# Optimization experiments

Measured on AMD Instinct MI355X. Metric: run time of the kernel, lower is better.

The kernel has to match this reference:

```python
import jax, jax.numpy as jnp
import numpy as np

D_MODEL = 1024
HEADS = 16
D_K = D_MODEL // HEADS
D_FF = 4096
B, S = 2, 2048
EPS = 1e-5


def setup_inputs() -> dict:
    key = jax.random.key(0)
    ks = jax.random.split(key, 16)
    sc_att = 1.0 / np.sqrt(D_MODEL)
    sc_ff1 = 1.0 / np.sqrt(D_MODEL)
    sc_ff2 = 1.0 / np.sqrt(D_FF)
    return {
        "input": jax.random.normal(ks[0], (B, S, D_MODEL), jnp.float32),
        "mask": jnp.ones((B, 1, 1, S), jnp.int32),
        # stacked per-head projections: [H, D_MODEL, D_K]
        "Wq": jax.random.normal(ks[1], (HEADS, D_MODEL, D_K), jnp.float32) * sc_att,
        "bq": jax.random.normal(ks[2], (HEADS, D_K), jnp.float32) * 0.01,
        "Wk": jax.random.normal(ks[3], (HEADS, D_MODEL, D_K), jnp.float32) * sc_att,
        "bk": jax.random.normal(ks[4], (HEADS, D_K), jnp.float32) * 0.01,
        "Wv": jax.random.normal(ks[5], (HEADS, D_MODEL, D_K), jnp.float32) * sc_att,
        "bv": jax.random.normal(ks[6], (HEADS, D_K), jnp.float32) * 0.01,
        "Wo": jax.random.normal(ks[7], (D_MODEL, D_MODEL), jnp.float32) * sc_att,
        "bo": jax.random.normal(ks[8], (D_MODEL,), jnp.float32) * 0.01,
        "ln1_g": jnp.ones((D_MODEL,), jnp.float32),
        "ln1_b": jnp.zeros((D_MODEL,), jnp.float32),
        "ln2_g": jnp.ones((D_MODEL,), jnp.float32),
        "ln2_b": jnp.zeros((D_MODEL,), jnp.float32),
        "W1": jax.random.normal(ks[9], (D_MODEL, D_FF), jnp.float32) * sc_ff1,
        "b1": jax.random.normal(ks[10], (D_FF,), jnp.float32) * 0.01,
        "W2": jax.random.normal(ks[11], (D_FF, D_MODEL), jnp.float32) * sc_ff2,
        "b2": jax.random.normal(ks[12], (D_MODEL,), jnp.float32) * 0.01,
    }


def _layernorm(x, g, b):
    mu = jnp.mean(x, axis=-1, keepdims=True)
    var = jnp.mean(jnp.square(x - mu), axis=-1, keepdims=True)
    return (x - mu) * jax.lax.rsqrt(var + EPS) * g + b


def reference(input, mask, Wq, bq, Wk, bk, Wv, bv, Wo, bo,
              ln1_g, ln1_b, ln2_g, ln2_b, W1, b1, W2, b2):
    x = input
    # per-head projections, stacked: [B,H,S,D_K]
    q = jnp.einsum('bsd,hdk->bhsk', x, Wq) + bq[None, :, None, :]
    k = jnp.einsum('bsd,hdk->bhsk', x, Wk) + bk[None, :, None, :]
    v = jnp.einsum('bsd,hdk->bhsk', x, Wv) + bv[None, :, None, :]
    scores = jnp.einsum('bhqk,bhsk->bhqs', q, k) / np.sqrt(D_K)  # [B,H,S,S]
    scores = jnp.where(mask == 0, jnp.float32(-1e9), scores)
    attn = jax.nn.softmax(scores, axis=-1)
    ctx = jnp.einsum('bhqs,bhsk->bhqk', attn, v)  # [B,H,S,D_K]
    # concat heads along feature dim (head h occupies slice h*D_K:(h+1)*D_K)
    ctx = jnp.transpose(ctx, (0, 2, 1, 3)).reshape(B, S, D_MODEL)
    att_out = ctx @ Wo + bo
    h = _layernorm(x + att_out, ln1_g, ln1_b)
    ff = jax.nn.relu(h @ W1 + b1) @ W2 + b2
    return _layernorm(h + ff, ln2_g, ln2_b)
```

## Files before the change

kernel.cpp:

```cpp
#include <hip/hip_runtime.h>
#include <cstdint>
#include <cstddef>

typedef unsigned short u16;
typedef unsigned int   u32;
typedef unsigned short u16x4 __attribute__((ext_vector_type(4)));
typedef unsigned short u16x8 __attribute__((ext_vector_type(8)));
typedef unsigned int   u32x2 __attribute__((ext_vector_type(2)));
typedef __bf16 bf16x8 __attribute__((ext_vector_type(8)));
typedef float f32x4 __attribute__((ext_vector_type(4)));

#define MFMA16(a, b, c) __builtin_amdgcn_mfma_f32_16x16x32_bf16((a), (b), (c), 0, 0, 0)

__device__ __forceinline__ float bf2f(u16 h) {
  union { unsigned u; float f; } v; v.u = ((unsigned)h) << 16; return v.f;
}
__device__ __forceinline__ u16 f2bf(float f) {
  union { float f; unsigned u; } v; v.f = f;
  unsigned r = v.u + 0x7fffu + ((v.u >> 16) & 1u);
  return (u16)(r >> 16);
}
__device__ __forceinline__ void gll16(const u16* g, u16* l) {
  __builtin_amdgcn_global_load_lds(
      (const __attribute__((address_space(1))) void*)g,
      (__attribute__((address_space(3))) void*)l, 16, 0, 0);
}
__device__ __forceinline__ float fast_exp2(float x) {
#if __has_builtin(__builtin_amdgcn_exp2f)
  return __builtin_amdgcn_exp2f(x);
#else
  return exp2f(x);
#endif
}

__global__ __launch_bounds__(256) void prep_all(
    const float* __restrict__ bq, const float* __restrict__ bk,
    const float* __restrict__ bv, const int* __restrict__ mask,
    float* __restrict__ biasq, float* __restrict__ madd2,
    const float* __restrict__ x, u16* __restrict__ xb,
    const float* __restrict__ Wq, const float* __restrict__ Wk,
    const float* __restrict__ Wv, u16* __restrict__ Wqkv_t,
    const float* __restrict__ Wo, const float* __restrict__ W1,
    const float* __restrict__ W2, u16* __restrict__ Wo_t,
    u16* __restrict__ W1_t, u16* __restrict__ W2_t) {
  __shared__ u16 tile[32][33];
  const int id = blockIdx.x;
  const int tid = threadIdx.x;

  if (id < 28) {
    int i = id * 256 + tid;
    if (i < 3072) {
      biasq[i] = (i < 1024) ? bq[i] * 0.18033688f
                            : (i < 2048 ? bk[i - 1024] : bv[i - 2048]);
    } else if (i < 7168) {
      int j = i - 3072;
      madd2[j] = mask[j] ? -23.083120f : -1.442695e9f;
    }
    return;
  }
  if (id < 4124) {
    int i = ((id - 28) * 256 + tid) * 4;
    const float4 v = *(const float4*)&x[i];
    u16x4 o;
    o[0] = f2bf(v.x); o[1] = f2bf(v.y); o[2] = f2bf(v.z); o[3] = f2bf(v.w);
    *(u16x4*)&xb[i] = o;
    return;
  }
  if (id < 7196) {
    int t = id - 4124;
    const int bx = t & 1, by = (t >> 1) & 31, z = t >> 6;
    const int which = z >> 4, h = z & 15;
    const float* in = (which == 0 ? Wq : (which == 1 ? Wk : Wv)) + (size_t)h * 1024 * 64;
    u16* out = Wqkv_t + ((size_t)which * 1024 + h * 64) * 1024;
    const float sc = (which == 0) ? 0.18033688f : 1.0f;
    const int tx = tid & 31, ty = tid >> 5;
    const int r0 = by * 32, c0 = bx * 32;
    #pragma unroll
    for (int i = 0; i < 32; i += 8)
      tile[ty + i][tx] = f2bf(in[(size_t)(r0 + ty + i) * 64 + c0 + tx] * sc);
    __syncthreads();
    #pragma unroll
    for (int i = 0; i < 32; i += 8)
      out[(size_t)(c0 + ty + i) * 1024 + r0 + tx] = tile[tx][ty + i];
    return;
  }
  {
    int t0 = id - 7196;
    const float* in; u16* outp; int R, C, cx, ry;
    if (t0 < 1024)      { in = Wo; outp = Wo_t; R = 1024; C = 1024; cx = t0 & 31;  ry = t0 >> 5; }
    else if (t0 < 5120) { int t = t0 - 1024; in = W1; outp = W1_t; R = 1024; C = 4096; cx = t & 127; ry = t >> 7; }
    else                { int t = t0 - 5120; in = W2; outp = W2_t; R = 4096; C = 1024; cx = t & 31;  ry = t >> 5; }
    const int tx = tid & 31, ty = tid >> 5;
    const int r0 = ry * 32, c0 = cx * 32;
    #pragma unroll
    for (int i = 0; i < 32; i += 8)
      tile[ty + i][tx] = f2bf(in[(size_t)(r0 + ty + i) * C + c0 + tx]);
    __syncthreads();
    #pragma unroll
    for (int i = 0; i < 32; i += 8)
      outp[(size_t)(c0 + ty + i) * R + r0 + tx] = tile[tx][ty + i];
  }
}

__device__ __forceinline__ void xcd_tiles(int& m0, int& n0) {
  const int gX = gridDim.x, gY = gridDim.y;
  int n = blockIdx.y * gX + blockIdx.x;
  int cpx = (gX * gY) >> 3;
  int t = (n & 7) * cpx + (n >> 3);
  n0 = (t / gY) * 128;
  m0 = (t % gY) * 128;
}

template <int MODE>
__global__ __launch_bounds__(256) void gemm_bt(
    const u16* __restrict__ A, const u16* __restrict__ Bt,
    const float* __restrict__ bias, u16* __restrict__ C,
    int M, int N, int K) {
  __shared__ __align__(16) u16 As[2][128 * 32];
  __shared__ __align__(16) u16 Bs[2][128 * 32];
  const int tid = threadIdx.x;
  const int lane = tid & 63;
  const int wave = tid >> 6;
  int m0, n0;
  xcd_tiles(m0, n0);
  const int wr = (wave >> 1) * 64;
  const int wc = (wave & 1) * 64;
  const int lrow = lane & 15;
  const int quad = lane >> 4;

  const int srow = lane >> 2;
  const int scol = (lane & 3) * 8;
  const u16* gA1 = &A[(size_t)(m0 + wave * 16 + srow) * K + scol];
  const u16* gA2 = &A[(size_t)(m0 + 64 + wave * 16 + srow) * K + scol];
  const u16* gB1 = &Bt[(size_t)(n0 + wave * 16 + srow) * K + scol];
  const u16* gB2 = &Bt[(size_t)(n0 + 64 + wave * 16 + srow) * K + scol];
  const int so1 = (wave * 16) * 32;
  const int so2 = (wave * 16 + 64) * 32;

  f32x4 acc[4][4];
  #pragma unroll
  for (int i = 0; i < 4; ++i)
    #pragma unroll
    for (int j = 0; j < 4; ++j)
      acc[i][j] = (f32x4){0.f, 0.f, 0.f, 0.f};

  for (int k0 = 0; k0 < K; k0 += 64) {
    gll16(gA1 + k0, &As[0][so1]);
    gll16(gA2 + k0, &As[0][so2]);
    gll16(gB1 + k0, &Bs[0][so1]);
    gll16(gB2 + k0, &Bs[0][so2]);
    gll16(gA1 + k0 + 32, &As[1][so1]);
    gll16(gA2 + k0 + 32, &As[1][so2]);
    gll16(gB1 + k0 + 32, &Bs[1][so1]);
    gll16(gB2 + k0 + 32, &Bs[1][so2]);
    __syncthreads();
    #pragma unroll
    for (int kb = 0; kb < 2; ++kb) {
      bf16x8 af[4], bfr[4];
      #pragma unroll
      for (int i = 0; i < 4; ++i) {
        af[i]  = *(const bf16x8*)&As[kb][(wr + i * 16 + lrow) * 32 + quad * 8];
        bfr[i] = *(const bf16x8*)&Bs[kb][(wc + i * 16 + lrow) * 32 + quad * 8];
      }
      #pragma unroll
      for (int fr = 0; fr < 4; ++fr)
        #pragma unroll
        for (int fc = 0; fc < 4; ++fc)
          acc[fr][fc] = MFMA16(af[fr], bfr[fc], acc[fr][fc]);
    }
    __syncthreads();
  }

  #pragma unroll
  for (int fr = 0; fr < 4; ++fr) {
    int rowb = m0 + wr + fr * 16 + quad * 4;
    #pragma unroll
    for (int fc = 0; fc < 4; ++fc) {
      int col = n0 + wc + fc * 16 + lrow;
      float bv = bias[col];
      #pragma unroll
      for (int r = 0; r < 4; ++r) {
        float v = acc[fr][fc][r] + bv;
        if (MODE == 1) v = fmaxf(v, 0.f);
        C[(size_t)(rowb + r) * N + col] = f2bf(v);
      }
    }
  }
}

__global__ __launch_bounds__(256) void gemm_splitk(
    const u16* __restrict__ A, const u16* __restrict__ Bt,
    u16* __restrict__ Cp, int M, int N, int K) {
  __shared__ __align__(16) u16 As[2][128 * 32];
  __shared__ __align__(16) u16 Bs[2][128 * 32];
  const int tid = threadIdx.x;
  const int lane = tid & 63;
  const int wave = tid >> 6;
  int m0, n0;
  xcd_tiles(m0, n0);
  const int kz = blockIdx.z;
  const int Kh = K >> 1;
  const int kbase = kz * Kh;
  const int wr = (wave >> 1) * 64;
  const int wc = (wave & 1) * 64;
  const int lrow = lane & 15;
  const int quad = lane >> 4;

  const int srow = lane >> 2;
  const int scol = (lane & 3) * 8;
  const u16* gA1 = &A[(size_t)(m0 + wave * 16 + srow) * K + kbase + scol];
  const u16* gA2 = &A[(size_t)(m0 + 64 + wave * 16 + srow) * K + kbase + scol];
  const u16* gB1 = &Bt[(size_t)(n0 + wave * 16 + srow) * K + kbase + scol];
  const u16* gB2 = &Bt[(size_t)(n0 + 64 + wave * 16 + srow) * K + kbase + scol];
  const int so1 = (wave * 16) * 32;
  const int so2 = (wave * 16 + 64) * 32;
  u16* C = Cp + (size_t)kz * M * N;

  f32x4 acc[4][4];
  #pragma unroll
  for (int i = 0; i < 4; ++i)
    #pragma unroll
    for (int j = 0; j < 4; ++j)
      acc[i][j] = (f32x4){0.f, 0.f, 0.f, 0.f};

  for (int k0 = 0; k0 < Kh; k0 += 64) {
    gll16(gA1 + k0, &As[0][so1]);
    gll16(gA2 + k0, &As[0][so2]);
    gll16(gB1 + k0, &Bs[0][so1]);
    gll16(gB2 + k0, &Bs[0][so2]);
    gll16(gA1 + k0 + 32, &As[1][so1]);
    gll16(gA2 + k0 + 32, &As[1][so2]);
    gll16(gB1 + k0 + 32, &Bs[1][so1]);
    gll16(gB2 + k0 + 32, &Bs[1][so2]);
    __syncthreads();
    #pragma unroll
    for (int kb = 0; kb < 2; ++kb) {
      bf16x8 af[4], bfr[4];
      #pragma unroll
      for (int i = 0; i < 4; ++i) {
        af[i]  = *(const bf16x8*)&As[kb][(wr + i * 16 + lrow) * 32 + quad * 8];
        bfr[i] = *(const bf16x8*)&Bs[kb][(wc + i * 16 + lrow) * 32 + quad * 8];
      }
      #pragma unroll
      for (int fr = 0; fr < 4; ++fr)
        #pragma unroll
        for (int fc = 0; fc < 4; ++fc)
          acc[fr][fc] = MFMA16(af[fr], bfr[fc], acc[fr][fc]);
    }
    __syncthreads();
  }

  #pragma unroll
  for (int fr = 0; fr < 4; ++fr) {
    int rowb = m0 + wr + fr * 16 + quad * 4;
    #pragma unroll
    for (int fc = 0; fc < 4; ++fc) {
      int col = n0 + wc + fc * 16 + lrow;
      #pragma unroll
      for (int r = 0; r < 4; ++r)
        C[(size_t)(rowb + r) * N + col] = f2bf(acc[fr][fc][r]);
    }
  }
}

__global__ __launch_bounds__(256) void attn_kernel(
    const u16* __restrict__ xqkv, const float* __restrict__ madd2,
    u16* __restrict__ ctx) {
  __shared__ __align__(16) u16 Ks[128][72];
  __shared__ __align__(16) u16 Vt[64][136];
  __shared__ __align__(16) u16 Ps[4][2][16][72];
  const int tid = threadIdx.x;
  const int lane = tid & 63;
  const int wave = tid >> 6;
  const int lrow = lane & 15;
  const int quad = lane >> 4;
  const int b = blockIdx.z, h = blockIdx.y;
  const int qb = blockIdx.x * 128 + wave * 16;
  const u16* Qp = xqkv + (size_t)b * 2048 * 3072 + h * 64;
  const u16* Kp = Qp + 1024;
  const u16* Vp = Qp + 2048;

  bf16x8 qa[2][2];
  #pragma unroll
  for (int t = 0; t < 2; ++t) {
    qa[t][0] = *(const bf16x8*)&Qp[(size_t)(qb + t * 64 + lrow) * 3072 + quad * 8];
    qa[t][1] = *(const bf16x8*)&Qp[(size_t)(qb + t * 64 + lrow) * 3072 + 32 + quad * 8];
  }

  f32x4 o[2][4];
  #pragma unroll
  for (int t = 0; t < 2; ++t)
    #pragma unroll
    for (int i = 0; i < 4; ++i) o[t][i] = (f32x4){0.f, 0.f, 0.f, 0.f};
  float rsum[2] = {0.f, 0.f};

  const int ks_row = tid >> 3, ks_col = (tid & 7) * 8;
  const int v_dg = tid >> 4;
  const int v_kp = tid & 15;
  const float* maddb = madd2 + b * 2048;

  u16x8 kreg[4];
  u16x4 va[4], vb[4];
  #pragma unroll
  for (int sh = 0; sh < 4; ++sh) {
    kreg[sh] = *(const u16x8*)&Kp[(size_t)(sh * 32 + ks_row) * 3072 + ks_col];
    va[sh] = *(const u16x4*)&Vp[(size_t)(sh * 32 + 2 * v_kp) * 3072 + v_dg * 4];
    vb[sh] = *(const u16x4*)&Vp[(size_t)(sh * 32 + 2 * v_kp + 1) * 3072 + v_dg * 4];
  }

  for (int s0 = 0; s0 < 2048; s0 += 128) {
    __syncthreads();
    #pragma unroll
    for (int sh = 0; sh < 4; ++sh) {
      *(u16x8*)&Ks[sh * 32 + ks_row][ks_col] = kreg[sh];
      #pragma unroll
      for (int j = 0; j < 4; ++j) {
        u32 pk = ((u32)vb[sh][j] << 16) | (u32)va[sh][j];
        *(u32*)&Vt[v_dg * 4 + j][sh * 32 + 2 * v_kp] = pk;
      }
    }
    __syncthreads();
    if (s0 + 128 < 2048) {
      #pragma unroll
      for (int sh = 0; sh < 4; ++sh) {
        int sb = s0 + 128 + sh * 32;
        kreg[sh] = *(const u16x8*)&Kp[(size_t)(sb + ks_row) * 3072 + ks_col];
        va[sh] = *(const u16x4*)&Vp[(size_t)(sb + 2 * v_kp) * 3072 + v_dg * 4];
        vb[sh] = *(const u16x4*)&Vp[(size_t)(sb + 2 * v_kp + 1) * 3072 + v_dg * 4];
      }
    }

    #pragma unroll
    for (int h2 = 0; h2 < 2; ++h2) {
      bf16x8 kf[4][2], vf[4][2];
      #pragma unroll
      for (int kb = 0; kb < 4; ++kb) {
        kf[kb][0] = *(const bf16x8*)&Ks[h2 * 64 + kb * 16 + lrow][quad * 8];
        kf[kb][1] = *(const bf16x8*)&Ks[h2 * 64 + kb * 16 + lrow][32 + quad * 8];
      }
      #pragma unroll
      for (int nb = 0; nb < 4; ++nb) {
        vf[nb][0] = *(const bf16x8*)&Vt[nb * 16 + lrow][(h2 * 2 + 0) * 32 + quad * 8];
        vf[nb][1] = *(const bf16x8*)&Vt[nb * 16 + lrow][(h2 * 2 + 1) * 32 + quad * 8];
      }

      #pragma unroll
      for (int t = 0; t < 2; ++t) {
        #pragma unroll
        for (int kb = 0; kb < 4; ++kb) {
          f32x4 z = (f32x4){0.f, 0.f, 0.f, 0.f};
          z = MFMA16(kf[kb][0], qa[t][0], z);
          z = MFMA16(kf[kb][1], qa[t][1], z);
          f32x4 m4 = *(const f32x4*)&maddb[s0 + h2 * 64 + kb * 16 + quad * 4];
          u32 pb[4];
          #pragma unroll
          for (int r = 0; r < 4; ++r) {
            float p = fast_exp2(z[r] + m4[r]);
            rsum[t] += p;
            union { float f; u32 u; } cv; cv.f = p;
            pb[r] = cv.u + 0x8000u;
          }
          u32x2 w2;
          w2[0] = __builtin_amdgcn_perm(pb[1], pb[0], 0x07060302);
          w2[1] = __builtin_amdgcn_perm(pb[3], pb[2], 0x07060302);
          *(u32x2*)&Ps[wave][t][lrow][kb * 16 + quad * 4] = w2;
        }
        #pragma unroll
        for (int kh = 0; kh < 2; ++kh) {
          bf16x8 pa = *(const bf16x8*)&Ps[wave][t][lrow][kh * 32 + quad * 8];
          #pragma unroll
          for (int nb = 0; nb < 4; ++nb)
            o[t][nb] = MFMA16(pa, vf[nb][kh], o[t][nb]);
        }
      }
    }
  }

  #pragma unroll
  for (int t = 0; t < 2; ++t) {
    float rs = rsum[t];
    rs += __shfl_xor(rs, 16, 64);
    rs += __shfl_xor(rs, 32, 64);
    float inv = 1.f / fmaxf(rs, 1e-30f);
    #pragma unroll
    for (int r = 0; r < 4; ++r) {
      float invq = __shfl(inv, quad * 4 + r, 64);
      int q = qb + t * 64 + quad * 4 + r;
      #pragma unroll
      for (int nb = 0; nb < 4; ++nb) {
        float v = o[t][nb][r] * invq;
        ctx[((size_t)b * 2048 + q) * 1024 + h * 64 + nb * 16 + lrow] = f2bf(v);
      }
    }
  }
}

template <int IN_BF, int OUT_BF>
__global__ __launch_bounds__(256) void add_ln2p(
    const void* __restrict__ xa_, const u16* __restrict__ p0,
    const u16* __restrict__ p1, const float* __restrict__ cb,
    const float* __restrict__ g, const float* __restrict__ bb,
    void* __restrict__ outp_) {
  __shared__ float red[8];
  const int tid = threadIdx.x;
  const size_t base = (size_t)blockIdx.x * 1024;
  const float* xf = (const float*)xa_;
  const u16*   xb = (const u16*)xa_;
  float v[4];
  float s = 0.f;
  #pragma unroll
  for (int i = 0; i < 4; ++i) {
    int c = i * 256 + tid;
    float xv = IN_BF ? bf2f(xb[base + c]) : xf[base + c];
    v[i] = xv + bf2f(p0[base + c]) + bf2f(p1[base + c]) + cb[c];
    s += v[i];
  }
  #pragma unroll
  for (int off = 32; off > 0; off >>= 1) s += __shfl_down(s, off, 64);
  if ((tid & 63) == 0) red[tid >> 6] = s;
  __syncthreads();
  float mean = (red[0] + red[1] + red[2] + red[3]) * (1.f / 1024.f);
  float s2 = 0.f;
  #pragma unroll
  for (int i = 0; i < 4; ++i) { float d = v[i] - mean; s2 += d * d; }
  #pragma unroll
  for (int off = 32; off > 0; off >>= 1) s2 += __shfl_down(s2, off, 64);
  if ((tid & 63) == 0) red[4 + (tid >> 6)] = s2;
  __syncthreads();
  float var = (red[4] + red[5] + red[6] + red[7]) * (1.f / 1024.f);
  float rstd = rsqrtf(var + 1e-5f);
  #pragma unroll
  for (int i = 0; i < 4; ++i) {
    int c = i * 256 + tid;
    float r = (v[i] - mean) * rstd * g[c] + bb[c];
    if (OUT_BF) ((u16*)outp_)[base + c] = f2bf(r);
    else        ((float*)outp_)[base + c] = r;
  }
}

extern "C" void kernel_launch(void* const* d_in, const int* in_sizes, int n_in,
                              void* d_out, int out_size, void* d_ws, size_t ws_size,
                              hipStream_t stream) {
  (void)in_sizes; (void)n_in; (void)out_size; (void)ws_size;
  const float* x    = (const float*)d_in[0];
  const int*   mask = (const int*)d_in[1];
  const float* Wq   = (const float*)d_in[2];
  const float* bq   = (const float*)d_in[3];
  const float* Wk   = (const float*)d_in[4];
  const float* bk   = (const float*)d_in[5];
  const float* Wv   = (const float*)d_in[6];
  const float* bv   = (const float*)d_in[7];
  const float* Wo   = (const float*)d_in[8];
  const float* bo   = (const float*)d_in[9];
  const float* ln1g = (const float*)d_in[10];
  const float* ln1b = (const float*)d_in[11];
  const float* ln2g = (const float*)d_in[12];
  const float* ln2b = (const float*)d_in[13];
  const float* W1   = (const float*)d_in[14];
  const float* b1   = (const float*)d_in[15];
  const float* W2   = (const float*)d_in[16];
  const float* b2   = (const float*)d_in[17];
  float* out = (float*)d_out;

  char* ws = (char*)d_ws;
  u16*   Wqkv_t = (u16*)(ws + 0);
  u16*   fp     = (u16*)(ws + 0);
  u16*   Wo_t   = (u16*)(ws + 6291456);
  u16*   W1_t   = (u16*)(ws + 8388608);
  u16*   W2_t   = (u16*)(ws + 16777216);
  u16*   xqkv   = (u16*)(ws + 25165824);
  u16*   wp     = (u16*)(ws + 25165824);
  u16*   xb     = (u16*)(ws + 50331648);
  u16*   ctx    = (u16*)(ws + 50331648);
  u16*   ff1    = (u16*)(ws + 25165824);
  u16*   hbuf   = (u16*)(ws + 67108864);
  float* biasq  = (float*)(ws + 75497472);
  float* madd2  = (float*)(ws + 75509760);

  prep_all<<<16412, 256, 0, stream>>>(bq, bk, bv, mask, biasq, madd2,
                                      x, xb, Wq, Wk, Wv, Wqkv_t,
                                      Wo, W1, W2, Wo_t, W1_t, W2_t);

  gemm_bt<0><<<dim3(24, 32), 256, 0, stream>>>(xb, Wqkv_t, biasq, xqkv,
                                               4096, 3072, 1024);
  attn_kernel<<<dim3(16, 16, 2), 256, 0, stream>>>(xqkv, madd2, ctx);
  gemm_splitk<<<dim3(8, 32, 2), 256, 0, stream>>>(ctx, Wo_t, wp, 4096, 1024, 1024);
  add_ln2p<0, 1><<<4096, 256, 0, stream>>>(x, wp, wp + 4194304, bo,
                                           ln1g, ln1b, hbuf);
  gemm_bt<1><<<dim3(32, 32), 256, 0, stream>>>(hbuf, W1_t, b1, ff1,
                                               4096, 4096, 1024);
  gemm_splitk<<<dim3(8, 32, 2), 256, 0, stream>>>(ff1, W2_t, fp, 4096, 1024, 4096);
  add_ln2p<1, 0><<<4096, 256, 0, stream>>>(hbuf, fp, fp + 4194304, b2,
                                           ln2g, ln2b, out);
}
```

Measured before the change: 411.2 us.

## Use 256x256 double-buffered GEMM tiles and shrink attention KV tile to 64

Replaces the 128x128 GEMM used for the QKV and FF1 projections with a 512-thread 256x256-tile kernel. It uses 128KB of dynamic LDS double-buffering, interleaves next-tile global-to-LDS loads with MFMA work under barriers, and uses fewer blocks. Separately, the attention kernel now streams K/V in 64-row chunks instead of 128, cutting LDS and register footprint at the cost of more synchronizations per pass. The large tiles raise data reuse but give fewer workgroups: 192 blocks for QKV, 256 for FF1, on a chip with 256 CUs. The 128KB of LDS per block may also limit occupancy.

Result: faster. 366.4 us (-10.9%).

```diff
diff --git a/kernel.cpp b/kernel.cpp
--- a/kernel.cpp
+++ b/kernel.cpp
@@ -110,69 +110,97 @@
   n0 = (t / gY) * 128;
   m0 = (t % gY) * 128;
 }
+__device__ __forceinline__ void xcd_tiles256(int& m0, int& n0) {
+  const int gX = gridDim.x, gY = gridDim.y;
+  int n = blockIdx.y * gX + blockIdx.x;
+  int cpx = (gX * gY) >> 3;
+  int t = (n & 7) * cpx + (n >> 3);
+  n0 = (t / gY) * 256;
+  m0 = (t % gY) * 256;
+}
 
 template <int MODE>
-__global__ __launch_bounds__(256) void gemm_bt(
+__global__ __launch_bounds__(512, 2) void gemm256(
     const u16* __restrict__ A, const u16* __restrict__ Bt,
     const float* __restrict__ bias, u16* __restrict__ C,
     int M, int N, int K) {
-  __shared__ __align__(16) u16 As[2][128 * 32];
-  __shared__ __align__(16) u16 Bs[2][128 * 32];
+  extern __shared__ __align__(16) u16 lds[];
+  u16* As = lds;
+  u16* Bs = lds + 2 * 256 * 64;
   const int tid = threadIdx.x;
-  const int lane = tid & 63;
-  const int wave = tid >> 6;
+  const int lane = tid & 63, wave = tid >> 6;
   int m0, n0;
-  xcd_tiles(m0, n0);
-  const int wr = (wave >> 1) * 64;
-  const int wc = (wave & 1) * 64;
-  const int lrow = lane & 15;
-  const int quad = lane >> 4;
-
-  const int srow = lane >> 2;
-  const int scol = (lane & 3) * 8;
-  const u16* gA1 = &A[(size_t)(m0 + wave * 16 + srow) * K + scol];
-  const u16* gA2 = &A[(size_t)(m0 + 64 + wave * 16 + srow) * K + scol];
-  const u16* gB1 = &Bt[(size_t)(n0 + wave * 16 + srow) * K + scol];
-  const u16* gB2 = &Bt[(size_t)(n0 + 64 + wave * 16 + srow) * K + scol];
-  const int so1 = (wave * 16) * 32;
-  const int so2 = (wave * 16 + 64) * 32;
-
-  f32x4 acc[4][4];
-  #pragma unroll
-  for (int i = 0; i < 4; ++i)
+  xcd_tiles256(m0, n0);
+  const int wr = (wave >> 2) * 128;
+  const int wc = (wave & 3) * 64;
+  const int lrow = lane & 15, quad = lane >> 4;
+
+  const int g_r = wave * 8 + (lane >> 3);
+  const int g_c = (lane & 7) * 8;
+  const u16* gA = A + (size_t)(m0 + g_r) * K + g_c;
+  const u16* gB = Bt + (size_t)(n0 + g_r) * K + g_c;
+  const int wbase = wave * 512;
+
+  f32x4 acc[8][4];
+  #pragma unroll
+  for (int i = 0; i < 8; ++i)
     #pragma unroll
     for (int j = 0; j < 4; ++j)
       acc[i][j] = (f32x4){0.f, 0.f, 0.f, 0.f};
 
-  for (int k0 = 0; k0 < K; k0 += 64) {
-    gll16(gA1 + k0, &As[0][so1]);
-    gll16(gA2 + k0, &As[0][so2]);
-    gll16(gB1 + k0, &Bs[0][so1]);
-    gll16(gB2 + k0, &Bs[0][so2]);
-    gll16(gA1 + k0 + 32, &As[1][so1]);
-    gll16(gA2 + k0 + 32, &As[1][so2]);
-    gll16(gB1 + k0 + 32, &Bs[1][so1]);
-    gll16(gB2 + k0 + 32, &Bs[1][so2]);
-    __syncthreads();
-    #pragma unroll
-    for (int kb = 0; kb < 2; ++kb) {
-      bf16x8 af[4], bfr[4];
-      #pragma unroll
-      for (int i = 0; i < 4; ++i) {
-        af[i]  = *(const bf16x8*)&As[kb][(wr + i * 16 + lrow) * 32 + quad * 8];
-        bfr[i] = *(const bf16x8*)&Bs[kb][(wc + i * 16 + lrow) * 32 + quad * 8];
-      }
-      #pragma unroll
-      for (int fr = 0; fr < 4; ++fr)
+  const int NT = K >> 6;
+
+  #pragma unroll
+  for (int h = 0; h < 2; ++h) {
+    gll16(gA + (size_t)(h * 128) * K,      As + h * 8192 + wbase);
+    gll16(gA + (size_t)(h * 128 + 64) * K, As + h * 8192 + 4096 + wbase);
+    gll16(gB + (size_t)(h * 128) * K,      Bs + h * 8192 + wbase);
+    gll16(gB + (size_t)(h * 128 + 64) * K, Bs + h * 8192 + 4096 + wbase);
+  }
+  __syncthreads();
+
+  for (int t = 0; t < NT; ++t) {
+    const int p = t & 1;
+    const u16* Ab = As + p * 16384;
+    const u16* Bb = Bs + p * 16384;
+    bf16x8 bfr[4][2];
+    #pragma unroll
+    for (int q = 0; q < 4; ++q) {
+      if (q == 0) {
         #pragma unroll
         for (int fc = 0; fc < 4; ++fc)
-          acc[fr][fc] = MFMA16(af[fr], bfr[fc], acc[fr][fc]);
-    }
-    __syncthreads();
-  }
-
-  #pragma unroll
-  for (int fr = 0; fr < 4; ++fr) {
+          #pragma unroll
+          for (int kh = 0; kh < 2; ++kh)
+            bfr[fc][kh] = *(const bf16x8*)&Bb[(wc + fc * 16 + lrow) * 64 + kh * 32 + quad * 8];
+      }
+      bf16x8 af2[2][2];
+      #pragma unroll
+      for (int j = 0; j < 2; ++j)
+        #pragma unroll
+        for (int kh = 0; kh < 2; ++kh)
+          af2[j][kh] = *(const bf16x8*)&Ab[(wr + (q * 2 + j) * 16 + lrow) * 64 + kh * 32 + quad * 8];
+      if (t + 1 < NT) {
+        const int kc = (t + 1) * 64;
+        u16* dst = ((q < 2) ? As : Bs) + (p ^ 1) * 16384 + (q & 1) * 8192 + wbase;
+        const u16* src = ((q < 2) ? gA : gB) + (size_t)((q & 1) * 128) * K + kc;
+        gll16(src, dst);
+        gll16(src + (size_t)64 * K, dst + 4096);
+      }
+      __builtin_amdgcn_s_barrier();
+      #pragma unroll
+      for (int j = 0; j < 2; ++j)
+        #pragma unroll
+        for (int fc = 0; fc < 4; ++fc) {
+          acc[q * 2 + j][fc] = MFMA16(af2[j][0], bfr[fc][0], acc[q * 2 + j][fc]);
+          acc[q * 2 + j][fc] = MFMA16(af2[j][1], bfr[fc][1], acc[q * 2 + j][fc]);
+        }
+      if (q < 3) __builtin_amdgcn_s_barrier();
+    }
+    __syncthreads();
+  }
+
+  #pragma unroll
+  for (int fr = 0; fr < 8; ++fr) {
     int rowb = m0 + wr + fr * 16 + quad * 4;
     #pragma unroll
     for (int fc = 0; fc < 4; ++fc) {
@@ -266,8 +294,8 @@
 __global__ __launch_bounds__(256) void attn_kernel(
     const u16* __restrict__ xqkv, const float* __restrict__ madd2,
     u16* __restrict__ ctx) {
-  __shared__ __align__(16) u16 Ks[128][72];
-  __shared__ __align__(16) u16 Vt[64][136];
+  __shared__ __align__(16) u16 Ks[64][72];
+  __shared__ __align__(16) u16 Vt[64][72];
   __shared__ __align__(16) u16 Ps[4][2][16][72];
   const int tid = threadIdx.x;
   const int lane = tid & 63;
@@ -299,19 +327,19 @@
   const int v_kp = tid & 15;
   const float* maddb = madd2 + b * 2048;
 
-  u16x8 kreg[4];
-  u16x4 va[4], vb[4];
-  #pragma unroll
-  for (int sh = 0; sh < 4; ++sh) {
+  u16x8 kreg[2];
+  u16x4 va[2], vb[2];
+  #pragma unroll
+  for (int sh = 0; sh < 2; ++sh) {
     kreg[sh] = *(const u16x8*)&Kp[(size_t)(sh * 32 + ks_row) * 3072 + ks_col];
     va[sh] = *(const u16x4*)&Vp[(size_t)(sh * 32 + 2 * v_kp) * 3072 + v_dg * 4];
     vb[sh] = *(const u16x4*)&Vp[(size_t)(sh * 32 + 2 * v_kp + 1) * 3072 + v_dg * 4];
   }
 
-  for (int s0 = 0; s0 < 2048; s0 += 128) {
-    __syncthreads();
-    #pragma unroll
-    for (int sh = 0; sh < 4; ++sh) {
+  for (int s0 = 0; s0 < 2048; s0 += 64) {
+    __syncthreads();
+    #pragma unroll
+    for (int sh = 0; sh < 2; ++sh) {
       *(u16x8*)&Ks[sh * 32 + ks_row][ks_col] = kreg[sh];
       #pragma unroll
       for (int j = 0; j < 4; ++j) {
@@ -320,58 +348,55 @@
       }
     }
     __syncthreads();
-    if (s0 + 128 < 2048) {
-      #pragma unroll
-      for (int sh = 0; sh < 4; ++sh) {
-        int sb = s0 + 128 + sh * 32;
+    if (s0 + 64 < 2048) {
+      #pragma unroll
+      for (int sh = 0; sh < 2; ++sh) {
+        int sb = s0 + 64 + sh * 32;
         kreg[sh] = *(const u16x8*)&Kp[(size_t)(sb + ks_row) * 3072 + ks_col];
         va[sh] = *(const u16x4*)&Vp[(size_t)(sb + 2 * v_kp) * 3072 + v_dg * 4];
         vb[sh] = *(const u16x4*)&Vp[(size_t)(sb + 2 * v_kp + 1) * 3072 + v_dg * 4];
       }
     }
 
-    #pragma unroll
-    for (int h2 = 0; h2 < 2; ++h2) {
-      bf16x8 kf[4][2], vf[4][2];
+    bf16x8 kf[4][2], vf[4][2];
+    #pragma unroll
+    for (int kb = 0; kb < 4; ++kb) {
+      kf[kb][0] = *(const bf16x8*)&Ks[kb * 16 + lrow][quad * 8];
+      kf[kb][1] = *(const bf16x8*)&Ks[kb * 16 + lrow][32 + quad * 8];
+    }
+    #pragma unroll
+    for (int nb = 0; nb < 4; ++nb) {
+      vf[nb][0] = *(const bf16x8*)&Vt[nb * 16 + lrow][quad * 8];
+      vf[nb][1] = *(const bf16x8*)&Vt[nb * 16 + lrow][32 + quad * 8];
+    }
+
+    #pragma unroll
+    for (int t = 0; t < 2; ++t) {
       #pragma unroll
       for (int kb = 0; kb < 4; ++kb) {
-        kf[kb][0] = *(const bf16x8*)&Ks[h2 * 64 + kb * 16 + lrow][quad * 8];
-        kf[kb][1] = *(const bf16x8*)&Ks[h2 * 64 + kb * 16 + lrow][32 + quad * 8];
-      }
-      #pragma unroll
-      for (int nb = 0; nb < 4; ++nb) {
-        vf[nb][0] = *(const bf16x8*)&Vt[nb * 16 + lrow][(h2 * 2 + 0) * 32 + quad * 8];
-        vf[nb][1] = *(const bf16x8*)&Vt[nb * 16 + lrow][(h2 * 2 + 1) * 32 + quad * 8];
-      }
-
-      #pragma unroll
-      for (int t = 0; t < 2; ++t) {
+        f32x4 z = (f32x4){0.f, 0.f, 0.f, 0.f};
+        z = MFMA16(kf[kb][0], qa[t][0], z);
+        z = MFMA16(kf[kb][1], qa[t][1], z);
+        f32x4 m4 = *(const f32x4*)&maddb[s0 + kb * 16 + quad * 4];
+        u32 pb[4];
         #pragma unroll
-        for (int kb = 0; kb < 4; ++kb) {
-          f32x4 z = (f32x4){0.f, 0.f, 0.f, 0.f};
-          z = MFMA16(kf[kb][0], qa[t][0], z);
-          z = MFMA16(kf[kb][1], qa[t][1], z);
-          f32x4 m4 = *(const f32x4*)&maddb[s0 + h2 * 64 + kb * 16 + quad * 4];
-          u32 pb[4];
-          #pragma unroll
-          for (int r = 0; r < 4; ++r) {
-            float p = fast_exp2(z[r] + m4[r]);
-            rsum[t] += p;
-            union { float f; u32 u; } cv; cv.f = p;
-            pb[r] = cv.u + 0x8000u;
-          }
-          u32x2 w2;
-          w2[0] = __builtin_amdgcn_perm(pb[1], pb[0], 0x07060302);
-          w2[1] = __builtin_amdgcn_perm(pb[3], pb[2], 0x07060302);
-          *(u32x2*)&Ps[wave][t][lrow][kb * 16 + quad * 4] = w2;
+        for (int r = 0; r < 4; ++r) {
+          float p = fast_exp2(z[r] + m4[r]);
+          rsum[t] += p;
+          union { float f; u32 u; } cv; cv.f = p;
+          pb[r] = cv.u + 0x8000u;
         }
+        u32x2 w2;
+        w2[0] = __builtin_amdgcn_perm(pb[1], pb[0], 0x07060302);
+        w2[1] = __builtin_amdgcn_perm(pb[3], pb[2], 0x07060302);
+        *(u32x2*)&Ps[wave][t][lrow][kb * 16 + quad * 4] = w2;
+      }
+      #pragma unroll
+      for (int kh = 0; kh < 2; ++kh) {
+        bf16x8 pa = *(const bf16x8*)&Ps[wave][t][lrow][kh * 32 + quad * 8];
         #pragma unroll
-        for (int kh = 0; kh < 2; ++kh) {
-          bf16x8 pa = *(const bf16x8*)&Ps[wave][t][lrow][kh * 32 + quad * 8];
-          #pragma unroll
-          for (int nb = 0; nb < 4; ++nb)
-            o[t][nb] = MFMA16(pa, vf[nb][kh], o[t][nb]);
-        }
+        for (int nb = 0; nb < 4; ++nb)
+          o[t][nb] = MFMA16(pa, vf[nb][kh], o[t][nb]);
       }
     }
   }
@@ -481,14 +506,14 @@
                                       x, xb, Wq, Wk, Wv, Wqkv_t,
                                       Wo, W1, W2, Wo_t, W1_t, W2_t);
 
-  gemm_bt<0><<<dim3(24, 32), 256, 0, stream>>>(xb, Wqkv_t, biasq, xqkv,
-                                               4096, 3072, 1024);
+  gemm256<0><<<dim3(12, 16), 512, 131072, stream>>>(xb, Wqkv_t, biasq, xqkv,
+                                                    4096, 3072, 1024);
   attn_kernel<<<dim3(16, 16, 2), 256, 0, stream>>>(xqkv, madd2, ctx);
   gemm_splitk<<<dim3(8, 32, 2), 256, 0, stream>>>(ctx, Wo_t, wp, 4096, 1024, 1024);
   add_ln2p<0, 1><<<4096, 256, 0, stream>>>(x, wp, wp + 4194304, bo,
                                            ln1g, ln1b, hbuf);
-  gemm_bt<1><<<dim3(32, 32), 256, 0, stream>>>(hbuf, W1_t, b1, ff1,
-                                               4096, 4096, 1024);
+  gemm256<1><<<dim3(16, 16), 512, 131072, stream>>>(hbuf, W1_t, b1, ff1,
+                                                    4096, 4096, 1024);
   gemm_splitk<<<dim3(8, 32, 2), 256, 0, stream>>>(ff1, W2_t, fp, 4096, 1024, 4096);
   add_ln2p<1, 0><<<4096, 256, 0, stream>>>(hbuf, fp, fp + 4194304, b2,
                                            ln2g, ln2b, out);
```
